# Kernel tuning notes

Measured on AMD Instinct MI355X. Metric: run time of the kernel, lower is better.

The kernel has to match this reference:

```python
import jax, jax.numpy as jnp
import numpy as np

B, S, F, H = 2, 2048, 2048, 16
DH = F // H  # head_dim = 128
ROPE_BASE = 10000.0


def apply_rope(x, offset):
    # x: [B, S, H, Dh]; rotate-half RoPE per head with positions offset..offset+S-1
    d = x.shape[-1]
    pos = jnp.arange(x.shape[1], dtype=jnp.float32) + offset          # [S]
    inv_freq = 1.0 / (ROPE_BASE ** (jnp.arange(0, d, 2, dtype=jnp.float32) / d))  # [Dh/2]
    ang = pos[:, None] * inv_freq[None, :]                             # [S, Dh/2]
    cos = jnp.cos(ang)[None, :, None, :].astype(x.dtype)               # [1,S,1,Dh/2]
    sin = jnp.sin(ang)[None, :, None, :].astype(x.dtype)
    x1, x2 = x[..., : d // 2], x[..., d // 2 :]
    return jnp.concatenate([x1 * cos - x2 * sin, x1 * sin + x2 * cos], axis=-1)


def setup_inputs() -> dict:
    key = jax.random.key(0)
    k0, k1, k2, k3 = jax.random.split(key, 4)
    lecun = (1.0 / F) ** 0.5
    in_q = jax.random.normal(k0, (B, S, F), dtype=jnp.float32)
    Wq = jax.random.normal(k1, (F, H, DH), dtype=jnp.float32) * lecun
    Wk = jax.random.normal(k2, (F, H, DH), dtype=jnp.float32) * lecun
    Wv = jax.random.normal(k3, (F, H, DH), dtype=jnp.float32) * lecun
    bq = jnp.zeros((H, DH), dtype=jnp.float32)
    bk = jnp.zeros((H, DH), dtype=jnp.float32)
    bv = jnp.zeros((H, DH), dtype=jnp.float32)
    mask = jnp.tril(jnp.ones((S, S), dtype=bool))[None, None, :, :]  # causal [1,1,S,S]
    return {"in_q": in_q, "Wq": Wq, "bq": bq, "Wk": Wk, "bk": bk,
            "Wv": Wv, "bv": bv, "mask": mask, "offset": 0}


def reference(in_q, Wq, bq, Wk, bk, Wv, bv, mask, offset):
    # QKV projections: LinearGeneral [B,S,F] x [F,H,Dh] -> [B,S,H,Dh]
    q = jnp.einsum("bsf,fhd->bshd", in_q, Wq) + bq
    k = jnp.einsum("bsf,fhd->bshd", in_q, Wk) + bk
    v = jnp.einsum("bsf,fhd->bshd", in_q, Wv) + bv
    # RoPE on q and k (merge/split-head reshape in original is a no-op on values)
    q = apply_rope(q, offset)
    k = apply_rope(k, offset)
    # dot-product attention
    scale = 1.0 / jnp.sqrt(jnp.asarray(DH, dtype=q.dtype))
    scores = jnp.einsum("bqhd,bkhd->bhqk", q, k) * scale   # [B,H,Sq,Skv]
    scores = jnp.where(mask, scores, jnp.finfo(scores.dtype).min)
    weights = jax.nn.softmax(scores, axis=-1)
    out = jnp.einsum("bhqk,bkhd->bqhd", weights, v)        # [B,S,H,Dh]
    return out.reshape(out.shape[0], out.shape[1], H * DH)  # merge heads
```

## Files before the change

### kernel.cpp

```cpp
#include <hip/hip_runtime.h>
#include <hip/hip_bf16.h>
#include <stdint.h>

#define NB 2
#define NS 2048
#define NFE 2048
#define NH 16
#define NDH 128

#define QSCALE (0.08838834764831845f * 1.4426950408889634f)

typedef __attribute__((ext_vector_type(4))) float f32x4;
typedef __attribute__((ext_vector_type(8))) __bf16 bf16x8;

__device__ __forceinline__ uint16_t f2bf(float f) {
  uint32_t u = __builtin_bit_cast(uint32_t, f);
  return (uint16_t)((u + 0x7fffu + ((u >> 16) & 1u)) >> 16);
}

__device__ __forceinline__ void gload_lds16(const void* g, void* l) {
  __builtin_amdgcn_global_load_lds((const __attribute__((address_space(1))) void*)g,
                                   (__attribute__((address_space(3))) void*)l,
                                   16, 0, 0);
}

#define MFMA16(a, b, c) __builtin_amdgcn_mfma_f32_16x16x32_bf16(a, b, c, 0, 0, 0)

__global__ void k_prep(const float* __restrict__ x, uint16_t* __restrict__ y,
                       float* __restrict__ cosT, float* __restrict__ sinT,
                       const int* __restrict__ offp,
                       const float* __restrict__ Wq, const float* __restrict__ Wk,
                       const float* __restrict__ Wv, uint16_t* __restrict__ Wt) {
  __shared__ uint16_t tile[64][65];
  int b = blockIdx.x;
  int t = threadIdx.x;
  if (b < 8192) {
    int i = (b * 256 + t) * 4;
    float4 v = *(const float4*)(x + i);
    ushort4 o;
    o.x = f2bf(v.x); o.y = f2bf(v.y); o.z = f2bf(v.z); o.w = f2bf(v.w);
    *(ushort4*)(y + i) = o;
  } else if (b < 8704) {
    int tid = (b - 8192) * 256 + t;
    int s = tid >> 6, i = tid & 63;
    float off = (float)offp[0];
    float inv = expf(-((float)i / 64.0f) * logf(10000.0f));
    float ang = ((float)s + off) * inv;
    cosT[tid] = cosf(ang);
    sinT[tid] = sinf(ang);
  } else {
    int idx = b - 8704;
    int which = idx >> 10, rem = idx & 1023;
    int k0 = (rem & 31) * 64, n0 = (rem >> 5) * 64;
    const float* Wsrc = (which == 0) ? Wq : ((which == 1) ? Wk : Wv);
#pragma unroll
    for (int it = 0; it < 4; ++it) {
      int vec = t + it * 256;
      int r = vec >> 4, c4 = vec & 15;
      float4 v = *(const float4*)&Wsrc[(size_t)(k0 + r) * NFE + n0 + c4 * 4];
      tile[r][c4 * 4 + 0] = f2bf(v.x);
      tile[r][c4 * 4 + 1] = f2bf(v.y);
      tile[r][c4 * 4 + 2] = f2bf(v.z);
      tile[r][c4 * 4 + 3] = f2bf(v.w);
    }
    __syncthreads();
#pragma unroll
    for (int it = 0; it < 4; ++it) {
      int vec = t + it * 256;
      int r = vec >> 4, c4 = vec & 15;
      ushort4 o;
      o.x = tile[c4 * 4 + 0][r];
      o.y = tile[c4 * 4 + 1][r];
      o.z = tile[c4 * 4 + 2][r];
      o.w = tile[c4 * 4 + 3][r];
      *(ushort4*)&Wt[(size_t)which * NFE * NFE + (size_t)(n0 + r) * NFE + k0 + c4 * 4] = o;
    }
  }
}

__global__ __launch_bounds__(256, 2) void k_gemm_qkv(
    const uint16_t* __restrict__ A, const uint16_t* __restrict__ Wt,
    const float* __restrict__ bq, const float* __restrict__ bk, const float* __restrict__ bv,
    const float* __restrict__ cosT, const float* __restrict__ sinT,
    uint16_t* __restrict__ qws, uint16_t* __restrict__ kws, uint16_t* __restrict__ vtws) {
  __shared__ alignas(16) uint16_t SM[2 * 128 * 64];
  uint16_t* Asm = SM;
  uint16_t* Bsm = SM + 8192;
  int mt = blockIdx.x;
  int nt = blockIdx.y;
  int which = nt >> 4, h = nt & 15;
  const uint16_t* Bsrc = Wt + (size_t)which * NFE * NFE + (size_t)h * NDH * NFE;
  const uint16_t* Arow = A + (size_t)mt * 128 * NFE;
  int t = threadIdx.x, w = t >> 6, l = t & 63;
  int g = l >> 4, c = l & 15;
  int wr = w >> 1, wc = w & 1;

  f32x4 acc[4][4];
#pragma unroll
  for (int m = 0; m < 4; ++m)
#pragma unroll
    for (int n = 0; n < 4; ++n) acc[m][n] = (f32x4){0.f, 0.f, 0.f, 0.f};

  for (int kt = 0; kt < NFE / 64; ++kt) {
    int k0 = kt * 64;
#pragma unroll
    for (int cc = 0; cc < 4; ++cc) {
      int flat = cc * 256 + t;
      int row = flat >> 3, sub = flat & 7;
      int scol = ((sub ^ (row & 7)) << 3) + k0;
      gload_lds16(&Arow[(size_t)row * NFE + scol], (char*)Asm + flat * 16);
    }
#pragma unroll
    for (int cc = 0; cc < 4; ++cc) {
      int flat = cc * 256 + t;
      int row = flat >> 3, sub = flat & 7;
      int scol = ((sub ^ (row & 7)) << 3) + k0;
      gload_lds16(&Bsrc[(size_t)row * NFE + scol], (char*)Bsm + flat * 16);
    }
    __syncthreads();
#pragma unroll
    for (int ks = 0; ks < 2; ++ks) {
      bf16x8 af[4], bf[4];
#pragma unroll
      for (int m = 0; m < 4; ++m) {
        int row = wr * 64 + m * 16 + c;
        int kb = ((ks * 32 + g * 8) * 2) ^ ((row & 7) << 4);
        af[m] = *(const bf16x8*)((const char*)Asm + row * 128 + kb);
      }
#pragma unroll
      for (int nf = 0; nf < 4; ++nf) {
        int row = wc * 32 + (nf & 1) * 16 + (nf >> 1) * 64 + c;
        int kb = ((ks * 32 + g * 8) * 2) ^ ((row & 7) << 4);
        bf[nf] = *(const bf16x8*)((const char*)Bsm + row * 128 + kb);
      }
#pragma unroll
      for (int m = 0; m < 4; ++m)
#pragma unroll
        for (int nf = 0; nf < 4; ++nf)
          acc[m][nf] = MFMA16(af[m], bf[nf], acc[m][nf]);
    }
    __syncthreads();
  }

  int mbase = mt * 128 + wr * 64;
  if (which < 2) {
    const float* bias = (which == 0) ? bq : bk;
    uint16_t* outp = (which == 0) ? qws : kws;
    float scl = (which == 0) ? QSCALE : 1.0f;
#pragma unroll
    for (int m = 0; m < 4; ++m)
#pragma unroll
      for (int np = 0; np < 2; ++np) {
        int i = wc * 32 + np * 16 + c;
        float b1 = bias[h * NDH + i], b2 = bias[h * NDH + 64 + i];
#pragma unroll
        for (int j = 0; j < 4; ++j) {
          int r = mbase + m * 16 + g * 4 + j;
          int bb = r >> 11, s = r & (NS - 1);
          float cs = cosT[(s << 6) + i], sn = sinT[(s << 6) + i];
          float x1 = acc[m][np][j] + b1;
          float x2 = acc[m][np + 2][j] + b2;
          uint16_t* op = outp + ((size_t)(bb * NH + h) * NS + s) * NDH;
          op[i] = f2bf((x1 * cs - x2 * sn) * scl);
          op[64 + i] = f2bf((x1 * sn + x2 * cs) * scl);
        }
      }
  } else {
#pragma unroll
    for (int m = 0; m < 4; ++m)
#pragma unroll
      for (int nf = 0; nf < 4; ++nf) {
        int d = wc * 32 + (nf & 1) * 16 + (nf >> 1) * 64 + c;
        float bv_ = bv[h * NDH + d];
#pragma unroll
        for (int j = 0; j < 4; j += 2) {
          int sp = wr * 64 + m * 16 + g * 4 + j;
          int idx = d * 128 + (sp ^ ((d & 7) << 3));
          uint32_t pk = (uint32_t)f2bf(acc[m][nf][j] + bv_) |
                        ((uint32_t)f2bf(acc[m][nf][j + 1] + bv_) << 16);
          *(uint32_t*)((char*)SM + (size_t)idx * 2) = pk;
        }
      }
    __syncthreads();
    int bb = mt >> 4;
    int s_base = (mt & 15) * 128;
    uint16_t* vtb = vtws + (size_t)(bb * NH + h) * NDH * NS;
#pragma unroll
    for (int it = 0; it < 8; ++it) {
      int flat = it * 256 + t;
      int d = flat >> 4, chunk = flat & 15;
      int s0 = chunk * 8;
      int idx = d * 128 + (s0 ^ ((d & 7) << 3));
      bf16x8 vv = *(const bf16x8*)((const char*)SM + (size_t)idx * 2);
      *(bf16x8*)(vtb + (size_t)d * NS + s_base + s0) = vv;
    }
  }
}

__global__ __launch_bounds__(256, 4) void k_attn(
    const uint16_t* __restrict__ qws, const uint16_t* __restrict__ kws,
    const uint16_t* __restrict__ vtws, float* __restrict__ out) {
  __shared__ alignas(16) uint16_t Ksm[2][64 * 128];
  __shared__ alignas(16) uint16_t Vsm[2][128 * 64];
  __shared__ alignas(16) uint16_t Psm[4][16 * 64];

  int bh = blockIdx.x;
  int t = threadIdx.x, w = t >> 6, l = t & 63;
  int g = l >> 4, c = l & 15;
  int bb = bh >> 4, h = bh & 15;

  const uint16_t* Qp = qws + (size_t)bh * NS * NDH;
  const uint16_t* Kp = kws + (size_t)bh * NS * NDH;
  const uint16_t* Vp = vtws + (size_t)bh * NDH * NS;

#define STAGE(bb_, kt_)                                                            \
  do {                                                                             \
    _Pragma("unroll") for (int cc = 0; cc < 4; ++cc) {                             \
      int flat = cc * 256 + t;                                                     \
      int row = flat >> 4, sub = flat & 15;                                        \
      int scol = ((sub ^ (row & 7)) << 3);                                         \
      gload_lds16(&Kp[(size_t)((kt_) * 64 + row) * NDH + scol],                    \
                  (char*)Ksm[bb_] + flat * 16);                                    \
    }                                                                              \
    _Pragma("unroll") for (int cc = 0; cc < 4; ++cc) {                             \
      int flat = cc * 256 + t;                                                     \
      int row = flat >> 3, sub = flat & 7;                                         \
      int scol = ((sub ^ (row & 7)) << 3);                                         \
      gload_lds16(&Vp[(size_t)row * NS + (kt_) * 64 + scol],                       \
                  (char*)Vsm[bb_] + flat * 16);                                    \
    }                                                                              \
  } while (0)

  for (int pass = 0; pass < 2; ++pass) {
    int y64 = pass ? (31 - blockIdx.y) : blockIdx.y;
    int q0 = y64 * 64;
    int r = q0 + w * 16 + c;

    bf16x8 qf[4];
#pragma unroll
    for (int kk = 0; kk < 4; ++kk)
      qf[kk] = *(const bf16x8*)&Qp[(size_t)r * NDH + kk * 32 + g * 8];

    f32x4 acc_o[8];
    float mreg = -1e30f, lreg = 0.f;
#pragma unroll
    for (int n = 0; n < 8; ++n) acc_o[n] = (f32x4){0.f, 0.f, 0.f, 0.f};

    int nkt = y64 + 1;
    STAGE(0, 0);
    __syncthreads();

    for (int kt = 0; kt < nkt; ++kt) {
      int cur = kt & 1;
      if (kt + 1 < nkt) STAGE(cur ^ 1, kt + 1);

      f32x4 sacc[4];
#pragma unroll
      for (int nf = 0; nf < 4; ++nf) sacc[nf] = (f32x4){0.f, 0.f, 0.f, 0.f};
#pragma unroll
      for (int kk = 0; kk < 4; ++kk) {
#pragma unroll
        for (int nf = 0; nf < 4; ++nf) {
          int row = nf * 16 + c;
          int kb = ((kk * 32 + g * 8) * 2) ^ ((row & 7) << 4);
          bf16x8 kfr = *(const bf16x8*)((const char*)Ksm[cur] + row * 256 + kb);
          sacc[nf] = MFMA16(kfr, qf[kk], sacc[nf]);
        }
      }

      if (kt == y64) {
#pragma unroll
        for (int nf = 0; nf < 4; ++nf)
#pragma unroll
          for (int j = 0; j < 4; ++j) {
            int kv = kt * 64 + nf * 16 + g * 4 + j;
            if (kv > r) sacc[nf][j] = -1e30f;
          }
      }

      float mx = -1e30f;
#pragma unroll
      for (int nf = 0; nf < 4; ++nf)
        mx = fmaxf(mx, fmaxf(fmaxf(sacc[nf][0], sacc[nf][1]),
                             fmaxf(sacc[nf][2], sacc[nf][3])));
      mx = fmaxf(mx, __shfl_xor(mx, 16));
      mx = fmaxf(mx, __shfl_xor(mx, 32));

      float mnew = mreg;
      if (!__all(mx <= mreg + 8.0f)) {
        mnew = fmaxf(mreg, mx);
        float alpha = exp2f(mreg - mnew);
        mreg = mnew;
        lreg *= alpha;
#pragma unroll
        for (int j = 0; j < 4; ++j) {
          float aj = __shfl(alpha, (l & 48) + g * 4 + j);
#pragma unroll
          for (int nf = 0; nf < 8; ++nf) acc_o[nf][j] *= aj;
        }
      }

      float rs = 0.f;
#pragma unroll
      for (int nf = 0; nf < 4; ++nf)
#pragma unroll
        for (int j = 0; j < 4; ++j) {
          float p = exp2f(sacc[nf][j] - mnew);
          sacc[nf][j] = p;
          rs += p;
        }
      rs += __shfl_xor(rs, 16);
      rs += __shfl_xor(rs, 32);
      lreg += rs;

#pragma unroll
      for (int nf = 0; nf < 4; ++nf) {
        uint32_t pk0 = (uint32_t)f2bf(sacc[nf][0]) | ((uint32_t)f2bf(sacc[nf][1]) << 16);
        uint32_t pk1 = (uint32_t)f2bf(sacc[nf][2]) | ((uint32_t)f2bf(sacc[nf][3]) << 16);
        int colb = (nf * 16 + g * 4) * 2;
        char* base = (char*)Psm[w] + c * 128;
        *(uint32_t*)(base + (colb ^ ((c & 7) << 4))) = pk0;
        *(uint32_t*)(base + ((colb + 4) ^ ((c & 7) << 4))) = pk1;
      }

#pragma unroll
      for (int kk2 = 0; kk2 < 2; ++kk2) {
        int prow = c;
        int pkb = ((kk2 * 32 + g * 8) * 2) ^ ((prow & 7) << 4);
        bf16x8 pf = *(const bf16x8*)((const char*)Psm[w] + prow * 128 + pkb);
#pragma unroll
        for (int nf = 0; nf < 8; ++nf) {
          int row = nf * 16 + c;
          int kb = ((kk2 * 32 + g * 8) * 2) ^ ((row & 7) << 4);
          bf16x8 vf = *(const bf16x8*)((const char*)Vsm[cur] + row * 128 + kb);
          acc_o[nf] = MFMA16(pf, vf, acc_o[nf]);
        }
      }
      __syncthreads();
    }

#pragma unroll
    for (int j = 0; j < 4; ++j) {
      float lj = __shfl(lreg, (l & 48) + g * 4 + j);
      float inv = 1.0f / lj;
      int s = q0 + w * 16 + g * 4 + j;
      float* op = out + ((size_t)(bb * NS + s)) * NFE + h * NDH;
#pragma unroll
      for (int nf = 0; nf < 8; ++nf) op[nf * 16 + c] = acc_o[nf][j] * inv;
    }
  }
#undef STAGE
}

extern "C" void kernel_launch(void* const* d_in, const int* in_sizes, int n_in,
                              void* d_out, int out_size, void* d_ws, size_t ws_size,
                              hipStream_t stream) {
  const float* in_q = (const float*)d_in[0];
  const float* Wq = (const float*)d_in[1];
  const float* bq = (const float*)d_in[2];
  const float* Wk = (const float*)d_in[3];
  const float* bk = (const float*)d_in[4];
  const float* Wv = (const float*)d_in[5];
  const float* bv = (const float*)d_in[6];
  const int* offp = (const int*)d_in[8];
  float* out = (float*)d_out;

  char* ws = (char*)d_ws;
  const size_t SZ_AQ = (size_t)4096 * 2048 * 2;
  const size_t SZ_WT = (size_t)3 * 2048 * 2048 * 2;
  const size_t SZ_TAB = (size_t)2048 * 64 * 4;
  const size_t SZ_QKV = (size_t)32 * 2048 * 128 * 2;
  uint16_t* Aq = (uint16_t*)(ws);
  uint16_t* Wt = (uint16_t*)(ws + SZ_AQ);
  float* cosT = (float*)(ws + SZ_AQ + SZ_WT);
  float* sinT = (float*)(ws + SZ_AQ + SZ_WT + SZ_TAB);
  uint16_t* qws = (uint16_t*)(ws + SZ_AQ + SZ_WT + 2 * SZ_TAB);
  uint16_t* kws = (uint16_t*)(ws + SZ_AQ + SZ_WT + 2 * SZ_TAB + SZ_QKV);
  uint16_t* vtws = (uint16_t*)(ws + SZ_AQ + SZ_WT + 2 * SZ_TAB + 2 * SZ_QKV);

  k_prep<<<11776, 256, 0, stream>>>(in_q, Aq, cosT, sinT, offp, Wq, Wk, Wv, Wt);
  k_gemm_qkv<<<dim3(32, 48), 256, 0, stream>>>(Aq, Wt, bq, bk, bv, cosT, sinT, qws, kws, vtws);
  k_attn<<<dim3(32, 16), 256, 0, stream>>>(qws, kws, vtws, out);
}
```

Measured before the change: 190.6 us.

## Fuse paired causal query tiles into one KV sweep sharing staged K/V

Replaces the two sequential passes (query tile y and 31-y) with a single KV loop that processes both query tiles at once. Each staged K/V tile is reused by both tiles, which halves global-to-LDS traffic for the low tile and removes a second pipeline prologue. The cost is doubled accumulator, Q-fragment and softmax-state registers, so launch bounds drop from 4 to 2 blocks per CU. Occupancy is lower and the Psm buffer is reused sequentially within an iteration.

```diff
diff --git a/kernel.cpp b/kernel.cpp
--- a/kernel.cpp
+++ b/kernel.cpp
@@ -197,7 +197,7 @@
   }
 }
 
-__global__ __launch_bounds__(256, 4) void k_attn(
+__global__ __launch_bounds__(256, 2) void k_attn(
     const uint16_t* __restrict__ qws, const uint16_t* __restrict__ kws,
     const uint16_t* __restrict__ vtws, float* __restrict__ out) {
   __shared__ alignas(16) uint16_t Ksm[2][64 * 128];
@@ -231,125 +231,125 @@
     }                                                                              \
   } while (0)
 
-  for (int pass = 0; pass < 2; ++pass) {
-    int y64 = pass ? (31 - blockIdx.y) : blockIdx.y;
-    int q0 = y64 * 64;
-    int r = q0 + w * 16 + c;
-
-    bf16x8 qf[4];
-#pragma unroll
-    for (int kk = 0; kk < 4; ++kk)
-      qf[kk] = *(const bf16x8*)&Qp[(size_t)r * NDH + kk * 32 + g * 8];
-
-    f32x4 acc_o[8];
-    float mreg = -1e30f, lreg = 0.f;
-#pragma unroll
-    for (int n = 0; n < 8; ++n) acc_o[n] = (f32x4){0.f, 0.f, 0.f, 0.f};
-
-    int nkt = y64 + 1;
-    STAGE(0, 0);
-    __syncthreads();
-
-    for (int kt = 0; kt < nkt; ++kt) {
-      int cur = kt & 1;
-      if (kt + 1 < nkt) STAGE(cur ^ 1, kt + 1);
-
-      f32x4 sacc[4];
-#pragma unroll
-      for (int nf = 0; nf < 4; ++nf) sacc[nf] = (f32x4){0.f, 0.f, 0.f, 0.f};
-#pragma unroll
-      for (int kk = 0; kk < 4; ++kk) {
-#pragma unroll
-        for (int nf = 0; nf < 4; ++nf) {
-          int row = nf * 16 + c;
-          int kb = ((kk * 32 + g * 8) * 2) ^ ((row & 7) << 4);
-          bf16x8 kfr = *(const bf16x8*)((const char*)Ksm[cur] + row * 256 + kb);
-          sacc[nf] = MFMA16(kfr, qf[kk], sacc[nf]);
-        }
-      }
-
-      if (kt == y64) {
-#pragma unroll
-        for (int nf = 0; nf < 4; ++nf)
-#pragma unroll
-          for (int j = 0; j < 4; ++j) {
-            int kv = kt * 64 + nf * 16 + g * 4 + j;
-            if (kv > r) sacc[nf][j] = -1e30f;
-          }
-      }
-
-      float mx = -1e30f;
-#pragma unroll
-      for (int nf = 0; nf < 4; ++nf)
-        mx = fmaxf(mx, fmaxf(fmaxf(sacc[nf][0], sacc[nf][1]),
-                             fmaxf(sacc[nf][2], sacc[nf][3])));
-      mx = fmaxf(mx, __shfl_xor(mx, 16));
-      mx = fmaxf(mx, __shfl_xor(mx, 32));
-
-      float mnew = mreg;
-      if (!__all(mx <= mreg + 8.0f)) {
-        mnew = fmaxf(mreg, mx);
-        float alpha = exp2f(mreg - mnew);
-        mreg = mnew;
-        lreg *= alpha;
-#pragma unroll
-        for (int j = 0; j < 4; ++j) {
-          float aj = __shfl(alpha, (l & 48) + g * 4 + j);
-#pragma unroll
-          for (int nf = 0; nf < 8; ++nf) acc_o[nf][j] *= aj;
-        }
-      }
-
-      float rs = 0.f;
-#pragma unroll
-      for (int nf = 0; nf < 4; ++nf)
-#pragma unroll
-        for (int j = 0; j < 4; ++j) {
-          float p = exp2f(sacc[nf][j] - mnew);
-          sacc[nf][j] = p;
-          rs += p;
-        }
-      rs += __shfl_xor(rs, 16);
-      rs += __shfl_xor(rs, 32);
-      lreg += rs;
-
-#pragma unroll
-      for (int nf = 0; nf < 4; ++nf) {
-        uint32_t pk0 = (uint32_t)f2bf(sacc[nf][0]) | ((uint32_t)f2bf(sacc[nf][1]) << 16);
-        uint32_t pk1 = (uint32_t)f2bf(sacc[nf][2]) | ((uint32_t)f2bf(sacc[nf][3]) << 16);
-        int colb = (nf * 16 + g * 4) * 2;
-        char* base = (char*)Psm[w] + c * 128;
-        *(uint32_t*)(base + (colb ^ ((c & 7) << 4))) = pk0;
-        *(uint32_t*)(base + ((colb + 4) ^ ((c & 7) << 4))) = pk1;
-      }
-
-#pragma unroll
-      for (int kk2 = 0; kk2 < 2; ++kk2) {
-        int prow = c;
-        int pkb = ((kk2 * 32 + g * 8) * 2) ^ ((prow & 7) << 4);
-        bf16x8 pf = *(const bf16x8*)((const char*)Psm[w] + prow * 128 + pkb);
-#pragma unroll
-        for (int nf = 0; nf < 8; ++nf) {
-          int row = nf * 16 + c;
-          int kb = ((kk2 * 32 + g * 8) * 2) ^ ((row & 7) << 4);
-          bf16x8 vf = *(const bf16x8*)((const char*)Vsm[cur] + row * 128 + kb);
-          acc_o[nf] = MFMA16(pf, vf, acc_o[nf]);
-        }
-      }
-      __syncthreads();
-    }
-
-#pragma unroll
-    for (int j = 0; j < 4; ++j) {
-      float lj = __shfl(lreg, (l & 48) + g * 4 + j);
-      float inv = 1.0f / lj;
-      int s = q0 + w * 16 + g * 4 + j;
-      float* op = out + ((size_t)(bb * NS + s)) * NFE + h * NDH;
-#pragma unroll
-      for (int nf = 0; nf < 8; ++nf) op[nf * 16 + c] = acc_o[nf][j] * inv;
-    }
+#define TILEBODY(qf_, acc_, mreg_, lreg_, y64_, r_)                                \
+  do {                                                                             \
+    f32x4 sacc[4];                                                                 \
+    _Pragma("unroll") for (int nf = 0; nf < 4; ++nf)                               \
+      sacc[nf] = (f32x4){0.f, 0.f, 0.f, 0.f};                                      \
+    _Pragma("unroll") for (int kk = 0; kk < 4; ++kk) {                             \
+      _Pragma("unroll") for (int nf = 0; nf < 4; ++nf) {                           \
+        int row = nf * 16 + c;                                                     \
+        int kb = ((kk * 32 + g * 8) * 2) ^ ((row & 7) << 4);                       \
+        bf16x8 kfr = *(const bf16x8*)((const char*)Ksm[cur] + row * 256 + kb);     \
+        sacc[nf] = MFMA16(kfr, qf_[kk], sacc[nf]);                                 \
+      }                                                                            \
+    }                                                                              \
+    if (kt == (y64_)) {                                                            \
+      _Pragma("unroll") for (int nf = 0; nf < 4; ++nf)                             \
+        _Pragma("unroll") for (int j = 0; j < 4; ++j) {                            \
+          int kv = kt * 64 + nf * 16 + g * 4 + j;                                  \
+          if (kv > (r_)) sacc[nf][j] = -1e30f;                                     \
+        }                                                                          \
+    }                                                                              \
+    float mx = -1e30f;                                                             \
+    _Pragma("unroll") for (int nf = 0; nf < 4; ++nf)                               \
+      mx = fmaxf(mx, fmaxf(fmaxf(sacc[nf][0], sacc[nf][1]),                        \
+                           fmaxf(sacc[nf][2], sacc[nf][3])));                      \
+    mx = fmaxf(mx, __shfl_xor(mx, 16));                                            \
+    mx = fmaxf(mx, __shfl_xor(mx, 32));                                            \
+    float mnew = mreg_;                                                            \
+    if (!__all(mx <= mreg_ + 8.0f)) {                                              \
+      mnew = fmaxf(mreg_, mx);                                                     \
+      float alpha = exp2f(mreg_ - mnew);                                           \
+      mreg_ = mnew;                                                                \
+      lreg_ *= alpha;                                                              \
+      _Pragma("unroll") for (int j = 0; j < 4; ++j) {                              \
+        float aj = __shfl(alpha, (l & 48) + g * 4 + j);                            \
+        _Pragma("unroll") for (int nf = 0; nf < 8; ++nf) acc_[nf][j] *= aj;        \
+      }                                                                            \
+    }                                                                              \
+    float rs = 0.f;                                                                \
+    _Pragma("unroll") for (int nf = 0; nf < 4; ++nf)                               \
+      _Pragma("unroll") for (int j = 0; j < 4; ++j) {                              \
+        float p = exp2f(sacc[nf][j] - mnew);                                       \
+        sacc[nf][j] = p;                                                           \
+        rs += p;                                                                   \
+      }                                                                            \
+    rs += __shfl_xor(rs, 16);                                                      \
+    rs += __shfl_xor(rs, 32);                                                      \
+    lreg_ += rs;                                                                   \
+    _Pragma("unroll") for (int nf = 0; nf < 4; ++nf) {                             \
+      uint32_t pk0 = (uint32_t)f2bf(sacc[nf][0]) | ((uint32_t)f2bf(sacc[nf][1]) << 16); \
+      uint32_t pk1 = (uint32_t)f2bf(sacc[nf][2]) | ((uint32_t)f2bf(sacc[nf][3]) << 16); \
+      int colb = (nf * 16 + g * 4) * 2;                                            \
+      char* base = (char*)Psm[w] + c * 128;                                        \
+      *(uint32_t*)(base + (colb ^ ((c & 7) << 4))) = pk0;                          \
+      *(uint32_t*)(base + ((colb + 4) ^ ((c & 7) << 4))) = pk1;                    \
+    }                                                                              \
+    _Pragma("unroll") for (int kk2 = 0; kk2 < 2; ++kk2) {                          \
+      int pkb = ((kk2 * 32 + g * 8) * 2) ^ ((c & 7) << 4);                         \
+      bf16x8 pf = *(const bf16x8*)((const char*)Psm[w] + c * 128 + pkb);           \
+      _Pragma("unroll") for (int nf = 0; nf < 8; ++nf) {                           \
+        int row = nf * 16 + c;                                                     \
+        int kb = ((kk2 * 32 + g * 8) * 2) ^ ((row & 7) << 4);                      \
+        bf16x8 vf = *(const bf16x8*)((const char*)Vsm[cur] + row * 128 + kb);      \
+        acc_[nf] = MFMA16(pf, vf, acc_[nf]);                                       \
+      }                                                                            \
+    }                                                                              \
+  } while (0)
+
+  int y64A = blockIdx.y;
+  int y64B = 31 - y64A;
+  int rA = y64A * 64 + w * 16 + c;
+  int rB = y64B * 64 + w * 16 + c;
+
+  bf16x8 qfA[4], qfB[4];
+#pragma unroll
+  for (int kk = 0; kk < 4; ++kk) {
+    qfA[kk] = *(const bf16x8*)&Qp[(size_t)rA * NDH + kk * 32 + g * 8];
+    qfB[kk] = *(const bf16x8*)&Qp[(size_t)rB * NDH + kk * 32 + g * 8];
+  }
+
+  f32x4 accA[8], accB[8];
+  float mA = -1e30f, lA = 0.f, mB = -1e30f, lB = 0.f;
+#pragma unroll
+  for (int n = 0; n < 8; ++n) {
+    accA[n] = (f32x4){0.f, 0.f, 0.f, 0.f};
+    accB[n] = (f32x4){0.f, 0.f, 0.f, 0.f};
+  }
+
+  STAGE(0, 0);
+  __syncthreads();
+
+  int ktB = y64B;
+  for (int kt = 0; kt <= ktB; ++kt) {
+    int cur = kt & 1;
+    if (kt < ktB) STAGE(cur ^ 1, kt + 1);
+    if (kt <= y64A) TILEBODY(qfA, accA, mA, lA, y64A, rA);
+    TILEBODY(qfB, accB, mB, lB, y64B, rB);
+    __syncthreads();
+  }
+
+#pragma unroll
+  for (int j = 0; j < 4; ++j) {
+    float lj = __shfl(lA, (l & 48) + g * 4 + j);
+    float inv = 1.0f / lj;
+    int s = y64A * 64 + w * 16 + g * 4 + j;
+    float* op = out + ((size_t)(bb * NS + s)) * NFE + h * NDH;
+#pragma unroll
+    for (int nf = 0; nf < 8; ++nf) op[nf * 16 + c] = accA[nf][j] * inv;
+  }
+#pragma unroll
+  for (int j = 0; j < 4; ++j) {
+    float lj = __shfl(lB, (l & 48) + g * 4 + j);
+    float inv = 1.0f / lj;
+    int s = y64B * 64 + w * 16 + g * 4 + j;
+    float* op = out + ((size_t)(bb * NS + s)) * NFE + h * NDH;
+#pragma unroll
+    for (int nf = 0; nf < 8; ++nf) op[nf * 16 + c] = accB[nf][j] * inv;
   }
 #undef STAGE
+#undef TILEBODY
 }
 
 extern "C" void kernel_launch(void* const* d_in, const int* in_sizes, int n_in,
```

Measured after the change: 186.2 us. -2.3%, faster.
